# Kernel optimization log

Hardware: AMD Instinct MI355X
Metric: run time of the kernel (lower is better)

Reference implementation:

```python
import jax, jax.numpy as jnp
import numpy as np

N_NODES = 50000
N_EDGES = 600000
HIDDEN = 128
EDGE_NF = 2          # concat([radial, edge_attr]) -> edges_in_d = 2
NORM_FACTOR = 100.0  # normalization_factor, aggregation 'sum'
NORM_CONSTANT = 1.0


def _lin(key, out_d, in_d):
    # xavier-ish init, (out, in) layout like torch.nn.Linear
    return jax.random.normal(key, (out_d, in_d), jnp.float32) * (1.0 / np.sqrt(in_d))


def setup_inputs() -> dict:
    key = jax.random.key(0)
    ks = iter(jax.random.split(key, 64))
    H = HIDDEN
    inp = {
        "h": jax.random.normal(next(ks), (N_NODES, H), jnp.float32),
        "x": jax.random.normal(next(ks), (N_NODES, 3), jnp.float32),
        "edge_attr": jax.random.normal(next(ks), (N_EDGES, 1), jnp.float32),
        "edge_index": jax.random.randint(next(ks), (2, N_EDGES), 0, N_NODES),
    }
    for i in range(2):  # two GCL layers
        inp[f"g{i}_ew1"] = _lin(next(ks), H, 2 * H + EDGE_NF)
        inp[f"g{i}_eb1"] = jnp.zeros((H,), jnp.float32)
        inp[f"g{i}_ew2"] = _lin(next(ks), H, H)
        inp[f"g{i}_eb2"] = jnp.zeros((H,), jnp.float32)
        inp[f"g{i}_aw"] = _lin(next(ks), 1, H)
        inp[f"g{i}_ab"] = jnp.zeros((1,), jnp.float32)
        inp[f"g{i}_nw1"] = _lin(next(ks), H, 2 * H)
        inp[f"g{i}_nb1"] = jnp.zeros((H,), jnp.float32)
        inp[f"g{i}_nw2"] = _lin(next(ks), H, H)
        inp[f"g{i}_nb2"] = jnp.zeros((H,), jnp.float32)
    inp["eq_w1"] = _lin(next(ks), H, 2 * H + EDGE_NF)
    inp["eq_b1"] = jnp.zeros((H,), jnp.float32)
    inp["eq_w2"] = _lin(next(ks), H, H)
    inp["eq_b2"] = jnp.zeros((H,), jnp.float32)
    inp["eq_w3"] = _lin(next(ks), 1, H)  # bias=False
    return inp


def reference(h, x, edge_attr, edge_index,
              g0_ew1, g0_eb1, g0_ew2, g0_eb2, g0_aw, g0_ab, g0_nw1, g0_nb1, g0_nw2, g0_nb2,
              g1_ew1, g1_eb1, g1_ew2, g1_eb2, g1_aw, g1_ab, g1_nw1, g1_nb1, g1_nw2, g1_nb2,
              eq_w1, eq_b1, eq_w2, eq_b2, eq_w3):
    silu = jax.nn.silu
    row, col = edge_index[0], edge_index[1]
    n = h.shape[0]

    # coord2diff
    diff = x[row] - x[col]                                   # [E, 3]
    radial = jnp.sum(diff * diff, axis=1, keepdims=True)     # [E, 1]
    norm = jnp.sqrt(radial + 1e-8)
    coord_diff = diff / (norm + NORM_CONSTANT)
    ea = jnp.concatenate([radial, edge_attr], axis=1)        # [E, 2]

    gcls = [
        (g0_ew1, g0_eb1, g0_ew2, g0_eb2, g0_aw, g0_ab, g0_nw1, g0_nb1, g0_nw2, g0_nb2),
        (g1_ew1, g1_eb1, g1_ew2, g1_eb2, g1_aw, g1_ab, g1_nw1, g1_nb1, g1_nw2, g1_nb2),
    ]
    for (ew1, eb1, ew2, eb2, aw, ab, nw1, nb1, nw2, nb2) in gcls:
        # edge model: gather -> MLP -> attention gate
        e_in = jnp.concatenate([h[row], h[col], ea], axis=1)  # [E, 2H+2]
        mij = silu(silu(e_in @ ew1.T + eb1) @ ew2.T + eb2)    # [E, H]
        att = jax.nn.sigmoid(mij @ aw.T + ab)                 # [E, 1]
        ef = mij * att
        # node model: scatter-add (sum agg, / normalization_factor)
        agg = jax.ops.segment_sum(ef, row, num_segments=n) / NORM_FACTOR
        msg = silu(jnp.concatenate([h, agg], axis=1) @ nw1.T + nb1) @ nw2.T + nb2
        h = h + msg

    # EquivariantUpdate (tanh=False)
    e_in = jnp.concatenate([h[row], h[col], ea], axis=1)
    s = silu(silu(e_in @ eq_w1.T + eq_b1) @ eq_w2.T + eq_b2) @ eq_w3.T  # [E, 1]
    trans = coord_diff * s                                              # [E, 3]
    x = x + jax.ops.segment_sum(trans, row, num_segments=n) / NORM_FACTOR
    return (h, x)
```

## Files before the change

kernel.cpp:

```cpp
#include <hip/hip_runtime.h>
#include <cmath>

typedef short bfv8 __attribute__((ext_vector_type(8)));
typedef float fv4  __attribute__((ext_vector_type(4)));

#define MFMA_B16(a,b,c) __builtin_amdgcn_mfma_f32_16x16x32_bf16((a),(b),(c),0,0,0)

__device__ __forceinline__ float siluf(float x) { return x / (1.0f + expf(-x)); }

__device__ __forceinline__ unsigned packsplit(float v) {
  unsigned uh = __float_as_uint(v) & 0xffff0000u;
  float lof = v - __uint_as_float(uh);
  return (uh >> 16) | (__float_as_uint(lof) & 0xffff0000u);
}

__device__ __forceinline__ unsigned bf16rne(float x) {
  unsigned u = __float_as_uint(x);
  return (u + 0x7fffu + ((u >> 16) & 1u)) >> 16;
}

__global__ void hist_kernel(const int* __restrict__ eidx, int E,
                            unsigned* __restrict__ cnt)
{
  const int e = blockIdx.x * 256 + threadIdx.x;
  if (e < E) atomicAdd(&cnt[eidx[e]], 1u);
}

__global__ void scan_kernel(const unsigned* __restrict__ cnt,
                            unsigned* __restrict__ cursor, int N)
{
  __shared__ unsigned part[1024];
  const int t = threadIdx.x;
  const int chunk = (N + 1023) / 1024;
  const int base = t * chunk;
  unsigned s = 0;
  for (int i = 0; i < chunk; ++i) {
    const int idx = base + i;
    if (idx < N) s += cnt[idx];
  }
  part[t] = s;
  __syncthreads();
  for (int off = 1; off < 1024; off <<= 1) {
    unsigned v = 0;
    if (t >= off) v = part[t - off];
    __syncthreads();
    if (t >= off) part[t] += v;
    __syncthreads();
  }
  unsigned pre = (t == 0) ? 0u : part[t - 1];
  for (int i = 0; i < chunk; ++i) {
    const int idx = base + i;
    if (idx < N) { cursor[idx] = pre; pre += cnt[idx]; }
  }
}

__global__ void scatter_kernel(const float* __restrict__ x,
                               const int* __restrict__ eidx,
                               const float* __restrict__ eattr, int E,
                               unsigned* __restrict__ cursor,
                               int* __restrict__ sRowA, int* __restrict__ sColA,
                               float* __restrict__ sRadA, float* __restrict__ sEaA)
{
  const int e = blockIdx.x * 256 + threadIdx.x;
  if (e >= E) return;
  const int r = eidx[e], c = eidx[E + e];
  const float dx = x[(size_t)r * 3 + 0] - x[(size_t)c * 3 + 0];
  const float dy = x[(size_t)r * 3 + 1] - x[(size_t)c * 3 + 1];
  const float dz = x[(size_t)r * 3 + 2] - x[(size_t)c * 3 + 2];
  const unsigned pos = atomicAdd(&cursor[r], 1u);
  sRowA[pos] = r;
  sColA[pos] = c;
  sRadA[pos] = dx * dx + dy * dy + dz * dz;
  sEaA[pos]  = eattr[e];
}

template <int MODE>
__global__ __launch_bounds__(256, 2)
void edge_mfma(const unsigned short* __restrict__ hhi,
               const unsigned short* __restrict__ hlo,
               const int* __restrict__ sRowA, const int* __restrict__ sColA,
               const float* __restrict__ sRadA, const float* __restrict__ sEaA,
               int E,
               const unsigned short* __restrict__ w1h, const unsigned short* __restrict__ w1l,
               const float* __restrict__ W1full, const float* __restrict__ b1,
               const unsigned short* __restrict__ w2h, const unsigned short* __restrict__ w2l,
               const float* __restrict__ b2,
               const float* __restrict__ awv, const float* __restrict__ abv,
               const float* __restrict__ xin,
               float* __restrict__ outbuf)
{
  extern __shared__ __align__(16) char smem[];
  unsigned* sHall  = (unsigned*)smem;
  unsigned* sStage = (unsigned*)(smem + 32768);
  char* ebase = smem + (MODE == 0 ? 65536 : 32768);
  int*   sRow = (int*)ebase;
  int*   sCol = sRow + 128;
  float* sRad = (float*)(sCol + 128);
  float* sEa  = sRad + 128;

  const int tid = threadIdx.x;
  const int w = tid >> 6, l = tid & 63;
  const int c16 = l & 15, g = l >> 4;
  const int e0 = blockIdx.x * 128;

  if (tid < 128) {
    const int e = min(e0 + tid, E - 1);
    sRow[tid] = sRowA[e];
    sCol[tid] = sColA[e];
    sRad[tid] = sRadA[e];
    sEa[tid]  = sEaA[e];
  }
  __syncthreads();

  const int rw = w * 32;
  int nidA[2], nidB[2];
#pragma unroll
  for (int rt = 0; rt < 2; ++rt) {
    nidA[rt] = sRow[rw + rt * 16 + c16];
    nidB[rt] = sCol[rw + rt * 16 + c16];
  }

  fv4 acc[2][8];
#pragma unroll
  for (int a = 0; a < 2; ++a)
#pragma unroll
    for (int b = 0; b < 8; ++b) acc[a][b] = (fv4)0.0f;

#pragma unroll 2
  for (int kc = 0; kc < 8; ++kc) {
    bfv8 Ah[2], Al[2];
    const int kh = (kc & 3) * 32 + g * 8;
#pragma unroll
    for (int rt = 0; rt < 2; ++rt) {
      const int nid = (kc < 4) ? nidA[rt] : nidB[rt];
      const size_t off = (size_t)nid * 128 + kh;
      Ah[rt] = *(const bfv8*)(hhi + off);
      Al[rt] = *(const bfv8*)(hlo + off);
    }
#pragma unroll
    for (int jt = 0; jt < 8; ++jt) {
      const size_t bo = ((size_t)(kc * 8 + jt) * 64 + l) * 8;
      bfv8 Bh = *(const bfv8*)(w1h + bo);
      bfv8 Bl = *(const bfv8*)(w1l + bo);
#pragma unroll
      for (int rt = 0; rt < 2; ++rt) {
        acc[rt][jt] = MFMA_B16(Ah[rt], Bh, acc[rt][jt]);
        acc[rt][jt] = MFMA_B16(Al[rt], Bh, acc[rt][jt]);
        acc[rt][jt] = MFMA_B16(Ah[rt], Bl, acc[rt][jt]);
      }
    }
  }

  unsigned* sHW = sHall + w * 2048;
  const float ab0 = (MODE == 0) ? abv[0] : 0.0f;

#pragma unroll 1
  for (int rt = 0; rt < 2; ++rt) {
#pragma unroll
    for (int jt = 0; jt < 8; ++jt) {
      const int col = jt * 16 + c16;
      const float wt0 = W1full[(size_t)col * 258 + 256];
      const float wt1 = W1full[(size_t)col * 258 + 257];
      const float bb  = b1[col];
#pragma unroll
      for (int reg = 0; reg < 4; ++reg) {
        const int rr = 4 * g + reg;
        const int er = rw + rt * 16 + rr;
        const float v = acc[rt][jt][reg] + sRad[er] * wt0 + sEa[er] * wt1 + bb;
        sHW[rr * 128 + (col ^ ((rr & 7) << 2))] = packsplit(siluf(v));
      }
    }

    fv4 accB[8];
#pragma unroll
    for (int jt = 0; jt < 8; ++jt) accB[jt] = (fv4)0.0f;
    const int sxz = (c16 & 7) << 2;
#pragma unroll 2
    for (int kc2 = 0; kc2 < 4; ++kc2) {
      const int k0 = kc2 * 32 + g * 8;
      const int i1 = c16 * 128 + (k0 ^ sxz);
      const int4 q0 = *((const int4*)(sHW + i1));
      const int4 q1 = *((const int4*)(sHW + (i1 ^ 4)));
      bfv8 Ah2, Al2;
      {
        const int qq[8] = {q0.x, q0.y, q0.z, q0.w, q1.x, q1.y, q1.z, q1.w};
#pragma unroll
        for (int i = 0; i < 8; ++i) {
          Ah2[i] = (short)(((unsigned)qq[i]) & 0xffffu);
          Al2[i] = (short)(((unsigned)qq[i]) >> 16);
        }
      }
#pragma unroll
      for (int jt = 0; jt < 8; ++jt) {
        const size_t bo = ((size_t)(kc2 * 8 + jt) * 64 + l) * 8;
        bfv8 Bh = *(const bfv8*)(w2h + bo);
        bfv8 Bl = *(const bfv8*)(w2l + bo);
        accB[jt] = MFMA_B16(Ah2, Bh, accB[jt]);
        accB[jt] = MFMA_B16(Al2, Bh, accB[jt]);
        accB[jt] = MFMA_B16(Ah2, Bl, accB[jt]);
      }
    }

    float p[4] = {0.f, 0.f, 0.f, 0.f};
#pragma unroll
    for (int jt = 0; jt < 8; ++jt) {
      const int col = jt * 16 + c16;
      const float bb = b2[col], aa = awv[col];
#pragma unroll
      for (int reg = 0; reg < 4; ++reg) {
        const float m = siluf(accB[jt][reg] + bb);
        accB[jt][reg] = m;
        p[reg] += m * aa;
      }
    }
#pragma unroll
    for (int msk = 1; msk < 16; msk <<= 1) {
#pragma unroll
      for (int reg = 0; reg < 4; ++reg) p[reg] += __shfl_xor(p[reg], msk, 64);
    }

    if constexpr (MODE == 0) {
      float att[4];
#pragma unroll
      for (int reg = 0; reg < 4; ++reg)
        att[reg] = 1.0f / (1.0f + expf(-(p[reg] + ab0)));
#pragma unroll
      for (int jt = 0; jt < 8; ++jt) {
#pragma unroll
        for (int reg = 0; reg < 4; ++reg) {
          const int er = rw + rt * 16 + 4 * g + reg;
          float v = (e0 + er < E) ? accB[jt][reg] * att[reg] : 0.0f;
          const float vn = __shfl_xor(v, 1, 64);
          if (!(c16 & 1)) {
            const int cp = jt * 8 + (c16 >> 1);
            sStage[er * 64 + (cp ^ (((er >> 2) & 3) << 3))] =
                bf16rne(v) | (bf16rne(vn) << 16);
          }
        }
      }
    } else {
      if (c16 == 0) {
#pragma unroll
        for (int reg = 0; reg < 4; ++reg) {
          const int er = rw + rt * 16 + 4 * g + reg;
          const int e = e0 + er;
          if (e < E) {
            const float s = p[reg] * 0.01f;
            const int nr = sRow[er], nc = sCol[er];
            const float dx = xin[(size_t)nr * 3 + 0] - xin[(size_t)nc * 3 + 0];
            const float dy = xin[(size_t)nr * 3 + 1] - xin[(size_t)nc * 3 + 1];
            const float dz = xin[(size_t)nr * 3 + 2] - xin[(size_t)nc * 3 + 2];
            const float inv = 1.0f / (sqrtf(dx * dx + dy * dy + dz * dz + 1e-8f) + 1.0f);
            unsafeAtomicAdd(outbuf + (size_t)nr * 3 + 0, dx * inv * s);
            unsafeAtomicAdd(outbuf + (size_t)nr * 3 + 1, dy * inv * s);
            unsafeAtomicAdd(outbuf + (size_t)nr * 3 + 2, dz * inv * s);
          }
        }
      }
    }
  }

  if constexpr (MODE == 0) {
    __syncthreads();
    const int cp = tid & 63;
    const int q  = tid >> 6;
    const int erb = q * 32;
    float a0 = 0.0f, a1 = 0.0f;
    int cur = sRow[erb];
#pragma unroll 4
    for (int i = 0; i < 32; ++i) {
      const int er = erb + i;
      const int r = sRow[er];
      if (r != cur) {
        if (a0 != 0.0f || a1 != 0.0f) {
          unsafeAtomicAdd(outbuf + (size_t)cur * 128 + 2 * cp,     a0);
          unsafeAtomicAdd(outbuf + (size_t)cur * 128 + 2 * cp + 1, a1);
        }
        cur = r; a0 = 0.0f; a1 = 0.0f;
      }
      const unsigned u = sStage[er * 64 + (cp ^ (((er >> 2) & 3) << 3))];
      a0 += __uint_as_float(u << 16);
      a1 += __uint_as_float(u & 0xffff0000u);
    }
    if (a0 != 0.0f || a1 != 0.0f) {
      unsafeAtomicAdd(outbuf + (size_t)cur * 128 + 2 * cp,     a0);
      unsafeAtomicAdd(outbuf + (size_t)cur * 128 + 2 * cp + 1, a1);
    }
  }
}

__global__ __launch_bounds__(256, 3)
void node_mfma(float* __restrict__ hio,
               const unsigned short* __restrict__ hhi,
               const unsigned short* __restrict__ hlo,
               const float* __restrict__ agg, int N,
               const unsigned short* __restrict__ w1h, const unsigned short* __restrict__ w1l,
               const float* __restrict__ b1,
               const unsigned short* __restrict__ w2h, const unsigned short* __restrict__ w2l,
               const float* __restrict__ b2)
{
  __shared__ __align__(16) unsigned sH[4][2048];

  const int tid = threadIdx.x;
  const int w = tid >> 6, l = tid & 63;
  const int c16 = l & 15, g = l >> 4;
  const int n0 = blockIdx.x * 128;
  const int rw = w * 32;

  int rowA[2];
#pragma unroll
  for (int rt = 0; rt < 2; ++rt) rowA[rt] = min(n0 + rw + rt * 16 + c16, N - 1);

  fv4 acc[2][8];
#pragma unroll
  for (int a = 0; a < 2; ++a)
#pragma unroll
    for (int b = 0; b < 8; ++b) acc[a][b] = (fv4)0.0f;

#pragma unroll 2
  for (int kc = 0; kc < 8; ++kc) {
    bfv8 Ah[2], Al[2];
    if (kc < 4) {
      const int kh = kc * 32 + g * 8;
#pragma unroll
      for (int rt = 0; rt < 2; ++rt) {
        const size_t off = (size_t)rowA[rt] * 128 + kh;
        Ah[rt] = *(const bfv8*)(hhi + off);
        Al[rt] = *(const bfv8*)(hlo + off);
      }
    } else {
      const int kh = (kc - 4) * 32 + g * 8;
#pragma unroll
      for (int rt = 0; rt < 2; ++rt) {
        const float4 v0 = *(const float4*)(agg + (size_t)rowA[rt] * 128 + kh);
        const float4 v1 = *(const float4*)(agg + (size_t)rowA[rt] * 128 + kh + 4);
        const float vv[8] = {v0.x, v0.y, v0.z, v0.w, v1.x, v1.y, v1.z, v1.w};
#pragma unroll
        for (int i = 0; i < 8; ++i) {
          const float xs = vv[i] * 0.01f;
          const unsigned uh = __float_as_uint(xs) & 0xffff0000u;
          Ah[rt][i] = (short)(uh >> 16);
          const float lof = xs - __uint_as_float(uh);
          Al[rt][i] = (short)(__float_as_uint(lof) >> 16);
        }
      }
    }
#pragma unroll
    for (int jt = 0; jt < 8; ++jt) {
      const size_t bo = ((size_t)(kc * 8 + jt) * 64 + l) * 8;
      bfv8 Bh = *(const bfv8*)(w1h + bo);
      bfv8 Bl = *(const bfv8*)(w1l + bo);
#pragma unroll
      for (int rt = 0; rt < 2; ++rt) {
        acc[rt][jt] = MFMA_B16(Ah[rt], Bh, acc[rt][jt]);
        acc[rt][jt] = MFMA_B16(Al[rt], Bh, acc[rt][jt]);
        acc[rt][jt] = MFMA_B16(Ah[rt], Bl, acc[rt][jt]);
      }
    }
  }

  unsigned* sHW = sH[w];
#pragma unroll 1
  for (int rt = 0; rt < 2; ++rt) {
#pragma unroll
    for (int jt = 0; jt < 8; ++jt) {
      const int col = jt * 16 + c16;
      const float bb = b1[col];
#pragma unroll
      for (int reg = 0; reg < 4; ++reg) {
        const int rr = 4 * g + reg;
        sHW[rr * 128 + (col ^ ((rr & 7) << 2))] = packsplit(siluf(acc[rt][jt][reg] + bb));
      }
    }

    fv4 accB[8];
#pragma unroll
    for (int jt = 0; jt < 8; ++jt) accB[jt] = (fv4)0.0f;
    const int sxz = (c16 & 7) << 2;
#pragma unroll 2
    for (int kc2 = 0; kc2 < 4; ++kc2) {
      const int k0 = kc2 * 32 + g * 8;
      const int i1 = c16 * 128 + (k0 ^ sxz);
      const int4 q0 = *((const int4*)(sHW + i1));
      const int4 q1 = *((const int4*)(sHW + (i1 ^ 4)));
      bfv8 Ah2, Al2;
      {
        const int qq[8] = {q0.x, q0.y, q0.z, q0.w, q1.x, q1.y, q1.z, q1.w};
#pragma unroll
        for (int i = 0; i < 8; ++i) {
          Ah2[i] = (short)(((unsigned)qq[i]) & 0xffffu);
          Al2[i] = (short)(((unsigned)qq[i]) >> 16);
        }
      }
#pragma unroll
      for (int jt = 0; jt < 8; ++jt) {
        const size_t bo = ((size_t)(kc2 * 8 + jt) * 64 + l) * 8;
        bfv8 Bh = *(const bfv8*)(w2h + bo);
        bfv8 Bl = *(const bfv8*)(w2l + bo);
        accB[jt] = MFMA_B16(Ah2, Bh, accB[jt]);
        accB[jt] = MFMA_B16(Al2, Bh, accB[jt]);
        accB[jt] = MFMA_B16(Ah2, Bl, accB[jt]);
      }
    }

#pragma unroll
    for (int reg = 0; reg < 4; ++reg) {
      const int n = n0 + rw + rt * 16 + 4 * g + reg;
      if (n < N) {
        float* hp = hio + (size_t)n * 128;
#pragma unroll
        for (int jt = 0; jt < 8; ++jt) {
          const int col = jt * 16 + c16;
          hp[col] += accB[jt][reg] + b2[col];
        }
      }
    }
  }
}

__global__ void split_kernel(const float* __restrict__ src,
                             unsigned short* __restrict__ hi,
                             unsigned short* __restrict__ lo, int n4)
{
  const int i = blockIdx.x * 256 + threadIdx.x;
  if (i >= n4) return;
  const float4 v = ((const float4*)src)[i];
  const float vv[4] = {v.x, v.y, v.z, v.w};
  ushort4 ho, lq;
  unsigned short* hp = (unsigned short*)&ho;
  unsigned short* lp = (unsigned short*)&lq;
#pragma unroll
  for (int k = 0; k < 4; ++k) {
    const unsigned uh = __float_as_uint(vv[k]) & 0xffff0000u;
    hp[k] = (unsigned short)(uh >> 16);
    const float lof = vv[k] - __uint_as_float(uh);
    lp[k] = (unsigned short)(__float_as_uint(lof) >> 16);
  }
  ((ushort4*)hi)[i] = ho;
  ((ushort4*)lo)[i] = lq;
}

struct WDesc { const float* src; unsigned short* hi; unsigned short* lo; int K; int SW; };
struct WAll { WDesc m[10]; };

__global__ void wprep_kernel(WAll wa)
{
  const WDesc d = wa.m[blockIdx.y];
  const int idx = blockIdx.x * 256 + threadIdx.x;
  const int j = idx & 127, k = idx >> 7;
  if (k >= d.K) return;
  const float v = d.src[(size_t)j * d.SW + k];
  const unsigned uh = __float_as_uint(v) & 0xffff0000u;
  const float lof = v - __uint_as_float(uh);
  const int fo = ((((k >> 5) * 8 + (j >> 4)) * 64) + ((k >> 3) & 3) * 16 + (j & 15)) * 8 + (k & 7);
  d.hi[fo] = (unsigned short)(uh >> 16);
  d.lo[fo] = (unsigned short)(__float_as_uint(lof) >> 16);
}

extern "C" void kernel_launch(void* const* d_in, const int* in_sizes, int n_in,
                              void* d_out, int out_size, void* d_ws, size_t ws_size,
                              hipStream_t stream)
{
  const float* h_in  = (const float*)d_in[0];
  const float* x_in  = (const float*)d_in[1];
  const float* eattr = (const float*)d_in[2];
  const int*   eidx  = (const int*)d_in[3];
  const int N = in_sizes[0] / 128;
  const int E = in_sizes[2];

  const float* P[25];
  for (int i = 0; i < 25; ++i) P[i] = (const float*)d_in[4 + i];

  float* h_out = (float*)d_out;
  float* x_out = (float*)d_out + (size_t)N * 128;

  float*    agg    = (float*)d_ws;
  unsigned* cnt    = (unsigned*)(agg + (size_t)N * 128);
  unsigned* cursor = cnt + N;
  int*      sRowA  = (int*)(cursor + N);
  int*      sColA  = sRowA + E;
  float*    sRadA  = (float*)(sColA + E);
  float*    sEaA   = sRadA + E;
  unsigned short* hhi = (unsigned short*)(sEaA + E);
  unsigned short* hlo = hhi + (size_t)N * 128;
  unsigned short* wptr = hlo + (size_t)N * 128;

  WAll wa;
  auto addw = [&](int slot, const float* s, int K, int SW) {
    wa.m[slot].src = s; wa.m[slot].hi = wptr; wa.m[slot].lo = wptr + (size_t)K * 128;
    wa.m[slot].K = K; wa.m[slot].SW = SW;
    wptr += (size_t)2 * K * 128;
  };
  addw(0, P[0], 256, 258);  addw(1, P[2], 128, 128);
  addw(2, P[6], 256, 256);  addw(3, P[8], 128, 128);
  addw(4, P[10], 256, 258); addw(5, P[12], 128, 128);
  addw(6, P[16], 256, 256); addw(7, P[18], 128, 128);
  addw(8, P[20], 256, 258); addw(9, P[22], 128, 128);

  hipMemcpyAsync(h_out, h_in, (size_t)N * 128 * sizeof(float),
                 hipMemcpyDeviceToDevice, stream);
  hipMemcpyAsync(x_out, x_in, (size_t)N * 3 * sizeof(float),
                 hipMemcpyDeviceToDevice, stream);

  hipMemsetAsync(cnt, 0, (size_t)N * sizeof(unsigned), stream);
  hist_kernel<<<(E + 255) / 256, 256, 0, stream>>>(eidx, E, cnt);
  scan_kernel<<<1, 1024, 0, stream>>>(cnt, cursor, N);
  scatter_kernel<<<(E + 255) / 256, 256, 0, stream>>>(x_in, eidx, eattr, E,
      cursor, sRowA, sColA, sRadA, sEaA);

  wprep_kernel<<<dim3(128, 10), 256, 0, stream>>>(wa);

  const int n4 = N * 32;
  const int sg = (n4 + 255) / 256;
  const int eg = (E + 127) / 128;
  const int ng = (N + 127) / 128;
  const int smem0 = 32768 + 32768 + 2048;
  const int smem1 = 32768 + 2048;

  for (int lyr = 0; lyr < 2; ++lyr) {
    const float* const* G = P + 10 * lyr;
    const WDesc* M = &wa.m[4 * lyr];
    split_kernel<<<sg, 256, 0, stream>>>(h_out, hhi, hlo, n4);
    hipMemsetAsync(agg, 0, (size_t)N * 128 * sizeof(float), stream);
    edge_mfma<0><<<eg, 256, smem0, stream>>>(hhi, hlo, sRowA, sColA, sRadA, sEaA, E,
        M[0].hi, M[0].lo, G[0], G[1], M[1].hi, M[1].lo, G[3],
        G[4], G[5], nullptr, agg);
    node_mfma<<<ng, 256, 0, stream>>>(h_out, hhi, hlo, agg, N,
        M[2].hi, M[2].lo, G[7], M[3].hi, M[3].lo, G[9]);
  }

  split_kernel<<<sg, 256, 0, stream>>>(h_out, hhi, hlo, n4);
  edge_mfma<1><<<eg, 256, smem1, stream>>>(hhi, hlo, sRowA, sColA, sRadA, sEaA, E,
      wa.m[8].hi, wa.m[8].lo, P[20], P[21], wa.m[9].hi, wa.m[9].lo, P[23],
      P[24], nullptr, x_in, x_out);
}
```

Before: 1.698 ms.

## Fuse h split into node kernel, register-reduce edge scatter, precompute coord diffs

The node kernel now writes the bf16 hi/lo split of the updated h directly, so the separate split_kernel runs only once instead of once per layer. The edge kernel drops its LDS bf16 staging pass and per-row run reduction. It now sums in fp32 registers across the 4 consecutive edges each lane holds when they share a row, then issues atomics. The normalized coord_diff is precomputed in the scatter pass, so the final edge kernel reads it instead of regathering x. Launch bounds rise to 4 blocks per CU and the inner loops are fully unrolled. The trade-off is more global atomics, because merging now covers only 4 edges instead of up to 32, plus extra register pressure.

```diff
diff --git a/kernel.cpp b/kernel.cpp
--- a/kernel.cpp
+++ b/kernel.cpp
@@ -12,11 +12,6 @@
   unsigned uh = __float_as_uint(v) & 0xffff0000u;
   float lof = v - __uint_as_float(uh);
   return (uh >> 16) | (__float_as_uint(lof) & 0xffff0000u);
-}
-
-__device__ __forceinline__ unsigned bf16rne(float x) {
-  unsigned u = __float_as_uint(x);
-  return (u + 0x7fffu + ((u >> 16) & 1u)) >> 16;
 }
 
 __global__ void hist_kernel(const int* __restrict__ eidx, int E,
@@ -59,7 +54,8 @@
                                const float* __restrict__ eattr, int E,
                                unsigned* __restrict__ cursor,
                                int* __restrict__ sRowA, int* __restrict__ sColA,
-                               float* __restrict__ sRadA, float* __restrict__ sEaA)
+                               float* __restrict__ sRadA, float* __restrict__ sEaA,
+                               float* __restrict__ sCdA)
 {
   const int e = blockIdx.x * 256 + threadIdx.x;
   if (e >= E) return;
@@ -67,36 +63,35 @@
   const float dx = x[(size_t)r * 3 + 0] - x[(size_t)c * 3 + 0];
   const float dy = x[(size_t)r * 3 + 1] - x[(size_t)c * 3 + 1];
   const float dz = x[(size_t)r * 3 + 2] - x[(size_t)c * 3 + 2];
+  const float rad = dx * dx + dy * dy + dz * dz;
+  const float inv = 1.0f / (sqrtf(rad + 1e-8f) + 1.0f);
   const unsigned pos = atomicAdd(&cursor[r], 1u);
   sRowA[pos] = r;
   sColA[pos] = c;
-  sRadA[pos] = dx * dx + dy * dy + dz * dz;
+  sRadA[pos] = rad;
   sEaA[pos]  = eattr[e];
+  sCdA[(size_t)pos * 3 + 0] = dx * inv;
+  sCdA[(size_t)pos * 3 + 1] = dy * inv;
+  sCdA[(size_t)pos * 3 + 2] = dz * inv;
 }
 
 template <int MODE>
-__global__ __launch_bounds__(256, 2)
+__global__ __launch_bounds__(256, 4)
 void edge_mfma(const unsigned short* __restrict__ hhi,
                const unsigned short* __restrict__ hlo,
                const int* __restrict__ sRowA, const int* __restrict__ sColA,
                const float* __restrict__ sRadA, const float* __restrict__ sEaA,
-               int E,
+               const float* __restrict__ sCdA, int E,
                const unsigned short* __restrict__ w1h, const unsigned short* __restrict__ w1l,
                const float* __restrict__ W1full, const float* __restrict__ b1,
                const unsigned short* __restrict__ w2h, const unsigned short* __restrict__ w2l,
                const float* __restrict__ b2,
                const float* __restrict__ awv, const float* __restrict__ abv,
-               const float* __restrict__ xin,
                float* __restrict__ outbuf)
 {
-  extern __shared__ __align__(16) char smem[];
-  unsigned* sHall  = (unsigned*)smem;
-  unsigned* sStage = (unsigned*)(smem + 32768);
-  char* ebase = smem + (MODE == 0 ? 65536 : 32768);
-  int*   sRow = (int*)ebase;
-  int*   sCol = sRow + 128;
-  float* sRad = (float*)(sCol + 128);
-  float* sEa  = sRad + 128;
+  __shared__ __align__(16) unsigned sHall[4][2048];
+  __shared__ int   sRow[128], sCol[128];
+  __shared__ float sRad[128], sEa[128];
 
   const int tid = threadIdx.x;
   const int w = tid >> 6, l = tid & 63;
@@ -126,7 +121,7 @@
 #pragma unroll
     for (int b = 0; b < 8; ++b) acc[a][b] = (fv4)0.0f;
 
-#pragma unroll 2
+#pragma unroll
   for (int kc = 0; kc < 8; ++kc) {
     bfv8 Ah[2], Al[2];
     const int kh = (kc & 3) * 32 + g * 8;
@@ -151,7 +146,7 @@
     }
   }
 
-  unsigned* sHW = sHall + w * 2048;
+  unsigned* sHW = sHall[w];
   const float ab0 = (MODE == 0) ? abv[0] : 0.0f;
 
 #pragma unroll 1
@@ -175,7 +170,7 @@
 #pragma unroll
     for (int jt = 0; jt < 8; ++jt) accB[jt] = (fv4)0.0f;
     const int sxz = (c16 & 7) << 2;
-#pragma unroll 2
+#pragma unroll
     for (int kc2 = 0; kc2 < 4; ++kc2) {
       const int k0 = kc2 * 32 + g * 8;
       const int i1 = c16 * 128 + (k0 ^ sxz);
@@ -219,80 +214,66 @@
       for (int reg = 0; reg < 4; ++reg) p[reg] += __shfl_xor(p[reg], msk, 64);
     }
 
+    const int base = rw + rt * 16 + 4 * g;
+    int rr4[4];
+#pragma unroll
+    for (int reg = 0; reg < 4; ++reg) rr4[reg] = sRow[base + reg];
+    const bool m01 = (rr4[0] == rr4[1]);
+    const bool m12 = (rr4[1] == rr4[2]);
+    const bool m23 = (rr4[2] == rr4[3]);
+
     if constexpr (MODE == 0) {
       float att[4];
 #pragma unroll
-      for (int reg = 0; reg < 4; ++reg)
-        att[reg] = 1.0f / (1.0f + expf(-(p[reg] + ab0)));
+      for (int reg = 0; reg < 4; ++reg) {
+        const float a = 1.0f / (1.0f + expf(-(p[reg] + ab0)));
+        att[reg] = (e0 + base + reg < E) ? a : 0.0f;
+      }
 #pragma unroll
       for (int jt = 0; jt < 8; ++jt) {
+        const int col = jt * 16 + c16;
+        const float v0 = accB[jt][0] * att[0];
+        const float v1 = accB[jt][1] * att[1];
+        const float v2 = accB[jt][2] * att[2];
+        const float v3 = accB[jt][3] * att[3];
+        const float p0 = v0;
+        const float p1 = v1 + (m01 ? p0 : 0.0f);
+        const float p2 = v2 + (m12 ? p1 : 0.0f);
+        const float p3 = v3 + (m23 ? p2 : 0.0f);
+        if (!m01) unsafeAtomicAdd(outbuf + (size_t)rr4[0] * 128 + col, p0);
+        if (!m12) unsafeAtomicAdd(outbuf + (size_t)rr4[1] * 128 + col, p1);
+        if (!m23) unsafeAtomicAdd(outbuf + (size_t)rr4[2] * 128 + col, p2);
+        unsafeAtomicAdd(outbuf + (size_t)rr4[3] * 128 + col, p3);
+      }
+    } else {
+      if (c16 < 3) {
+        const int cx = c16;
+        float v[4];
 #pragma unroll
         for (int reg = 0; reg < 4; ++reg) {
-          const int er = rw + rt * 16 + 4 * g + reg;
-          float v = (e0 + er < E) ? accB[jt][reg] * att[reg] : 0.0f;
-          const float vn = __shfl_xor(v, 1, 64);
-          if (!(c16 & 1)) {
-            const int cp = jt * 8 + (c16 >> 1);
-            sStage[er * 64 + (cp ^ (((er >> 2) & 3) << 3))] =
-                bf16rne(v) | (bf16rne(vn) << 16);
-          }
+          const int e = min(e0 + base + reg, E - 1);
+          const float s = (e0 + base + reg < E) ? p[reg] * 0.01f : 0.0f;
+          v[reg] = sCdA[(size_t)e * 3 + cx] * s;
         }
-      }
-    } else {
-      if (c16 == 0) {
-#pragma unroll
-        for (int reg = 0; reg < 4; ++reg) {
-          const int er = rw + rt * 16 + 4 * g + reg;
-          const int e = e0 + er;
-          if (e < E) {
-            const float s = p[reg] * 0.01f;
-            const int nr = sRow[er], nc = sCol[er];
-            const float dx = xin[(size_t)nr * 3 + 0] - xin[(size_t)nc * 3 + 0];
-            const float dy = xin[(size_t)nr * 3 + 1] - xin[(size_t)nc * 3 + 1];
-            const float dz = xin[(size_t)nr * 3 + 2] - xin[(size_t)nc * 3 + 2];
-            const float inv = 1.0f / (sqrtf(dx * dx + dy * dy + dz * dz + 1e-8f) + 1.0f);
-            unsafeAtomicAdd(outbuf + (size_t)nr * 3 + 0, dx * inv * s);
-            unsafeAtomicAdd(outbuf + (size_t)nr * 3 + 1, dy * inv * s);
-            unsafeAtomicAdd(outbuf + (size_t)nr * 3 + 2, dz * inv * s);
-          }
-        }
-      }
-    }
-  }
-
-  if constexpr (MODE == 0) {
-    __syncthreads();
-    const int cp = tid & 63;
-    const int q  = tid >> 6;
-    const int erb = q * 32;
-    float a0 = 0.0f, a1 = 0.0f;
-    int cur = sRow[erb];
-#pragma unroll 4
-    for (int i = 0; i < 32; ++i) {
-      const int er = erb + i;
-      const int r = sRow[er];
-      if (r != cur) {
-        if (a0 != 0.0f || a1 != 0.0f) {
-          unsafeAtomicAdd(outbuf + (size_t)cur * 128 + 2 * cp,     a0);
-          unsafeAtomicAdd(outbuf + (size_t)cur * 128 + 2 * cp + 1, a1);
-        }
-        cur = r; a0 = 0.0f; a1 = 0.0f;
-      }
-      const unsigned u = sStage[er * 64 + (cp ^ (((er >> 2) & 3) << 3))];
-      a0 += __uint_as_float(u << 16);
-      a1 += __uint_as_float(u & 0xffff0000u);
-    }
-    if (a0 != 0.0f || a1 != 0.0f) {
-      unsafeAtomicAdd(outbuf + (size_t)cur * 128 + 2 * cp,     a0);
-      unsafeAtomicAdd(outbuf + (size_t)cur * 128 + 2 * cp + 1, a1);
-    }
-  }
-}
-
-__global__ __launch_bounds__(256, 3)
+        const float p0 = v[0];
+        const float p1 = v[1] + (m01 ? p0 : 0.0f);
+        const float p2 = v[2] + (m12 ? p1 : 0.0f);
+        const float p3 = v[3] + (m23 ? p2 : 0.0f);
+        if (!m01) unsafeAtomicAdd(outbuf + (size_t)rr4[0] * 3 + cx, p0);
+        if (!m12) unsafeAtomicAdd(outbuf + (size_t)rr4[1] * 3 + cx, p1);
+        if (!m23) unsafeAtomicAdd(outbuf + (size_t)rr4[2] * 3 + cx, p2);
+        unsafeAtomicAdd(outbuf + (size_t)rr4[3] * 3 + cx, p3);
+      }
+    }
+  }
+}
+
+__global__ __launch_bounds__(256, 4)
 void node_mfma(float* __restrict__ hio,
                const unsigned short* __restrict__ hhi,
                const unsigned short* __restrict__ hlo,
+               unsigned short* __restrict__ ohi,
+               unsigned short* __restrict__ olo,
                const float* __restrict__ agg, int N,
                const unsigned short* __restrict__ w1h, const unsigned short* __restrict__ w1l,
                const float* __restrict__ b1,
@@ -317,7 +298,7 @@
 #pragma unroll
     for (int b = 0; b < 8; ++b) acc[a][b] = (fv4)0.0f;
 
-#pragma unroll 2
+#pragma unroll
   for (int kc = 0; kc < 8; ++kc) {
     bfv8 Ah[2], Al[2];
     if (kc < 4) {
@@ -377,7 +358,7 @@
 #pragma unroll
     for (int jt = 0; jt < 8; ++jt) accB[jt] = (fv4)0.0f;
     const int sxz = (c16 & 7) << 2;
-#pragma unroll 2
+#pragma unroll
     for (int kc2 = 0; kc2 < 4; ++kc2) {
       const int k0 = kc2 * 32 + g * 8;
       const int i1 = c16 * 128 + (k0 ^ sxz);
@@ -411,7 +392,11 @@
 #pragma unroll
         for (int jt = 0; jt < 8; ++jt) {
           const int col = jt * 16 + c16;
-          hp[col] += accB[jt][reg] + b2[col];
+          const float nv = hp[col] + accB[jt][reg] + b2[col];
+          hp[col] = nv;
+          const unsigned ps = packsplit(nv);
+          ohi[(size_t)n * 128 + col] = (unsigned short)(ps & 0xffffu);
+          olo[(size_t)n * 128 + col] = (unsigned short)(ps >> 16);
         }
       }
     }
@@ -481,7 +466,8 @@
   int*      sColA  = sRowA + E;
   float*    sRadA  = (float*)(sColA + E);
   float*    sEaA   = sRadA + E;
-  unsigned short* hhi = (unsigned short*)(sEaA + E);
+  float*    sCdA   = sEaA + E;
+  unsigned short* hhi = (unsigned short*)(sCdA + (size_t)3 * E);
   unsigned short* hlo = hhi + (size_t)N * 128;
   unsigned short* wptr = hlo + (size_t)N * 128;
 
@@ -506,7 +492,7 @@
   hist_kernel<<<(E + 255) / 256, 256, 0, stream>>>(eidx, E, cnt);
   scan_kernel<<<1, 1024, 0, stream>>>(cnt, cursor, N);
   scatter_kernel<<<(E + 255) / 256, 256, 0, stream>>>(x_in, eidx, eattr, E,
-      cursor, sRowA, sColA, sRadA, sEaA);
+      cursor, sRowA, sColA, sRadA, sEaA, sCdA);
 
   wprep_kernel<<<dim3(128, 10), 256, 0, stream>>>(wa);
 
@@ -514,23 +500,21 @@
   const int sg = (n4 + 255) / 256;
   const int eg = (E + 127) / 128;
   const int ng = (N + 127) / 128;
-  const int smem0 = 32768 + 32768 + 2048;
-  const int smem1 = 32768 + 2048;
+
+  split_kernel<<<sg, 256, 0, stream>>>(h_out, hhi, hlo, n4);
 
   for (int lyr = 0; lyr < 2; ++lyr) {
     const float* const* G = P + 10 * lyr;
     const WDesc* M = &wa.m[4 * lyr];
-    split_kernel<<<sg, 256, 0, stream>>>(h_out, hhi, hlo, n4);
     hipMemsetAsync(agg, 0, (size_t)N * 128 * sizeof(float), stream);
-    edge_mfma<0><<<eg, 256, smem0, stream>>>(hhi, hlo, sRowA, sColA, sRadA, sEaA, E,
+    edge_mfma<0><<<eg, 256, 0, stream>>>(hhi, hlo, sRowA, sColA, sRadA, sEaA, sCdA, E,
         M[0].hi, M[0].lo, G[0], G[1], M[1].hi, M[1].lo, G[3],
-        G[4], G[5], nullptr, agg);
-    node_mfma<<<ng, 256, 0, stream>>>(h_out, hhi, hlo, agg, N,
+        G[4], G[5], agg);
+    node_mfma<<<ng, 256, 0, stream>>>(h_out, hhi, hlo, hhi, hlo, agg, N,
         M[2].hi, M[2].lo, G[7], M[3].hi, M[3].lo, G[9]);
   }
 
-  split_kernel<<<sg, 256, 0, stream>>>(h_out, hhi, hlo, n4);
-  edge_mfma<1><<<eg, 256, smem1, stream>>>(hhi, hlo, sRowA, sColA, sRadA, sEaA, E,
+  edge_mfma<1><<<eg, 256, 0, stream>>>(hhi, hlo, sRowA, sColA, sRadA, sEaA, sCdA, E,
       wa.m[8].hi, wa.m[8].lo, P[20], P[21], wa.m[9].hi, wa.m[9].lo, P[23],
-      P[24], nullptr, x_in, x_out);
-}
+      P[24], nullptr, x_out);
+}
```

After: 4.604 ms. +171.1%, slower.
